# Kernel tuning notes

Measured on AMD Instinct MI355X. Metric: run time of the kernel, lower is better.

The kernel has to match this reference:

```python
import jax, jax.numpy as jnp
import numpy as np
from jax import lax

H_STEP = 1.0 / 3.0  # h = (t1 - t0) / N with t0=0, t1=1, N=3
N_STEPS = 3


def _conv(x, w):
    # x: [B, C, H, W], w: [O, I, kh, kw], 'same' padding, stride 1
    return lax.conv_general_dilated(
        x, w, window_strides=(1, 1), padding='SAME',
        dimension_numbers=('NCHW', 'OIHW', 'NCHW'))


def setup_inputs() -> dict:
    key = jax.random.key(0)
    ks = jax.random.split(key, 5)
    B, C, H, W = 16, 128, 128, 128
    fan_in = C * 9
    return {
        'x': jax.random.normal(ks[0], (B, C, H, W), dtype=jnp.float32),
        'w1': jax.random.normal(ks[1], (C, C, 3, 3), dtype=jnp.float32) * (2.0 / fan_in) ** 0.5,
        'b1': jax.random.normal(ks[2], (C,), dtype=jnp.float32) * 0.01,
        'w2': jax.random.normal(ks[3], (C, C, 3, 3), dtype=jnp.float32) * (2.0 / fan_in) ** 0.5,
        'b2': jax.random.normal(ks[4], (C,), dtype=jnp.float32) * 0.01,
    }


def reference(x, w1, b1, w2, b2):
    # Euler-step residual block: x <- x + h * conv2(relu(conv1(x))) for N steps
    for _ in range(N_STEPS):
        t = jax.nn.relu(_conv(x, w1) + b1[None, :, None, None])
        x = x + H_STEP * (_conv(t, w2) + b2[None, :, None, None])
    return jax.nn.relu(x)
```

## Files before the change

### kernel.cpp

```cpp
#include <hip/hip_runtime.h>
#include <hip/hip_bf16.h>


#define BATCH 16
#define CH    128
#define HH    128
#define WW    128
#define H_STEP (1.0f/3.0f)

#define CI_PAD 136

typedef short bf16x8 __attribute__((ext_vector_type(8)));
typedef float f32x4  __attribute__((ext_vector_type(4)));

__device__ __forceinline__ float bf2f(unsigned short u) {
    union { unsigned int i; float f; } c; c.i = ((unsigned int)u) << 16; return c.f;
}
__device__ __forceinline__ unsigned short f2bf(float f) {
    union { float f; unsigned int i; } c; c.f = f;
    unsigned int i = c.i;
    return (unsigned short)((i + 0x7FFFu + ((i >> 16) & 1u)) >> 16);
}

__global__ __launch_bounds__(256)
void transpose_x(const float* __restrict__ x, unsigned short* __restrict__ xb)
{
    __shared__ unsigned short s[128 * 132];
    const int tid = threadIdx.x;
    const int bz  = blockIdx.x;
    const int b = bz >> 7, y = bz & 127;

    #pragma unroll
    for (int it = 0; it < 16; ++it) {
        int idx = it * 256 + tid;
        int ci = idx >> 5, xq = idx & 31;
        float4 v = *(const float4*)&x[(((size_t)b * CH + ci) * HH + y) * WW + xq * 4];
        uint2 p;
        p.x = (unsigned int)f2bf(v.x) | ((unsigned int)f2bf(v.y) << 16);
        p.y = (unsigned int)f2bf(v.z) | ((unsigned int)f2bf(v.w) << 16);
        *(uint2*)&s[ci * 132 + xq * 4] = p;
    }
    __syncthreads();
    #pragma unroll
    for (int it = 0; it < 8; ++it) {
        int idx = it * 256 + tid;
        int xx = idx >> 4, cc = idx & 15;
        unsigned short t[8];
        #pragma unroll
        for (int k = 0; k < 8; ++k) t[k] = s[(cc * 8 + k) * 132 + xx];
        uint4 p;
        p.x = (unsigned int)t[0] | ((unsigned int)t[1] << 16);
        p.y = (unsigned int)t[2] | ((unsigned int)t[3] << 16);
        p.z = (unsigned int)t[4] | ((unsigned int)t[5] << 16);
        p.w = (unsigned int)t[6] | ((unsigned int)t[7] << 16);
        *(uint4*)&xb[((size_t)(b * HH + y) * WW + xx) * CH + cc * 8] = p;
    }
}

__global__ __launch_bounds__(256)
void convert_w(const float* __restrict__ w, unsigned short* __restrict__ wb)
{
    int idx = blockIdx.x * 256 + threadIdx.x;
    #pragma unroll
    for (int t = 0; t < 9; ++t)
        wb[t * 16384 + idx] = f2bf(w[(size_t)idx * 9 + t]);
}

template<int MODE>
__global__ __launch_bounds__(256, 2)
void conv_mfma(const unsigned short* __restrict__ in,
               const unsigned short* __restrict__ wb,
               const float* __restrict__ bias,
               const unsigned short* resb,
               unsigned short* outb,
               float* __restrict__ outf)
{
    __shared__ unsigned short s_in[130 * CI_PAD];
    __shared__ unsigned short s_w [128 * CI_PAD];

    const int tid = threadIdx.x;
    const int bz  = blockIdx.x;
    const int b = bz >> 7, y = bz & 127;

    const int lane = tid & 63;
    const int wid  = tid >> 6;
    const int woc0 = (wid >> 1) * 64;
    const int wpx0 = (wid & 1) * 64;
    const int n16  = lane & 15;
    const int q    = lane >> 4;

    f32x4 acc[4][4];
    #pragma unroll
    for (int i = 0; i < 4; ++i)
        #pragma unroll
        for (int j = 0; j < 4; ++j) acc[i][j] = (f32x4)0.0f;

    if (tid < 34) {
        int r  = (tid < 17) ? 0 : 129;
        int cc = (tid < 17) ? tid : tid - 17;
        uint4 z = {0u, 0u, 0u, 0u};
        *(uint4*)&s_in[r * CI_PAD + cc * 8] = z;
    }

    for (int ky = 0; ky < 3; ++ky) {
        const int gy = y + ky - 1;
        if (gy < 0 || gy >= HH) continue;
        const size_t inrow = ((size_t)(b * HH + gy) * WW) * CH;

        for (int kx = 0; kx < 3; ++kx) {
            __syncthreads();
            if (kx == 0) {
                #pragma unroll
                for (int it = 0; it < 8; ++it) {
                    int idx = it * 256 + tid;
                    int x = idx >> 4, cc = idx & 15;
                    uint4 v = *(const uint4*)&in[inrow + (size_t)x * CH + cc * 8];
                    *(uint4*)&s_in[(x + 1) * CI_PAD + cc * 8] = v;
                }
            }
            const unsigned short* wt = wb + (ky * 3 + kx) * 16384;
            #pragma unroll
            for (int it = 0; it < 8; ++it) {
                int idx = it * 256 + tid;
                int oc = idx >> 4, cc = idx & 15;
                uint4 v = *(const uint4*)&wt[oc * 128 + cc * 8];
                *(uint4*)&s_w[oc * CI_PAD + cc * 8] = v;
            }
            __syncthreads();

            #pragma unroll
            for (int c0 = 0; c0 < 128; c0 += 32) {
                bf16x8 af[4], bfr[4];
                #pragma unroll
                for (int i = 0; i < 4; ++i)
                    af[i] = *(const bf16x8*)&s_w[(woc0 + i * 16 + n16) * CI_PAD + c0 + q * 8];
                #pragma unroll
                for (int j = 0; j < 4; ++j)
                    bfr[j] = *(const bf16x8*)&s_in[(wpx0 + j * 16 + n16 + kx) * CI_PAD + c0 + q * 8];
                #pragma unroll
                for (int i = 0; i < 4; ++i)
                    #pragma unroll
                    for (int j = 0; j < 4; ++j)
                        acc[i][j] = __builtin_amdgcn_mfma_f32_16x16x32_bf16(
                            af[i], bfr[j], acc[i][j], 0, 0, 0);
            }
        }
    }

    const int ybase = (b * HH + y) * WW;
    if (MODE == 0 || MODE == 1) {
        #pragma unroll
        for (int j = 0; j < 4; ++j) {
            int x = wpx0 + j * 16 + n16;
            size_t pbase = (size_t)(ybase + x) * CH;
            #pragma unroll
            for (int i = 0; i < 4; ++i) {
                int oc0 = woc0 + i * 16 + q * 4;
                float v0 = acc[i][j][0] + bias[oc0 + 0];
                float v1 = acc[i][j][1] + bias[oc0 + 1];
                float v2 = acc[i][j][2] + bias[oc0 + 2];
                float v3 = acc[i][j][3] + bias[oc0 + 3];
                if (MODE == 0) {
                    v0 = fmaxf(v0, 0.f); v1 = fmaxf(v1, 0.f);
                    v2 = fmaxf(v2, 0.f); v3 = fmaxf(v3, 0.f);
                } else {
                    uint2 rr = *(const uint2*)&resb[pbase + oc0];
                    v0 = bf2f((unsigned short)(rr.x & 0xffff)) + H_STEP * v0;
                    v1 = bf2f((unsigned short)(rr.x >> 16))    + H_STEP * v1;
                    v2 = bf2f((unsigned short)(rr.y & 0xffff)) + H_STEP * v2;
                    v3 = bf2f((unsigned short)(rr.y >> 16))    + H_STEP * v3;
                }
                uint2 po;
                po.x = (unsigned int)f2bf(v0) | ((unsigned int)f2bf(v1) << 16);
                po.y = (unsigned int)f2bf(v2) | ((unsigned int)f2bf(v3) << 16);
                *(uint2*)&outb[pbase + oc0] = po;
            }
        }
    } else {
        #pragma unroll
        for (int i = 0; i < 4; ++i) {
            #pragma unroll
            for (int r = 0; r < 4; ++r) {
                int oc = woc0 + i * 16 + q * 4 + r;
                float bv = bias[oc];
                size_t orow = ((size_t)(b * CH + oc) * HH + y) * WW;
                #pragma unroll
                for (int j = 0; j < 4; ++j) {
                    int x = wpx0 + j * 16 + n16;
                    float v = acc[i][j][r] + bv;
                    v = bf2f(resb[(size_t)(ybase + x) * CH + oc]) + H_STEP * v;
                    outf[orow + x] = fmaxf(v, 0.f);
                }
            }
        }
    }
}

extern "C" void kernel_launch(void* const* d_in, const int* in_sizes, int n_in,
                              void* d_out, int out_size, void* d_ws, size_t ws_size,
                              hipStream_t stream) {
    const float* x0 = (const float*)d_in[0];
    const float* w1 = (const float*)d_in[1];
    const float* b1 = (const float*)d_in[2];
    const float* w2 = (const float*)d_in[3];
    const float* b2 = (const float*)d_in[4];

    const size_t NELEM = (size_t)BATCH * CH * HH * WW;
    unsigned short* XB = (unsigned short*)d_ws;
    unsigned short* T  = XB + NELEM;

    unsigned short* WB1;
    if (ws_size >= NELEM * 4 + 2 * 294912)
        WB1 = T + NELEM;
    else
        WB1 = (unsigned short*)d_in[0];
    unsigned short* WB2 = WB1 + 9 * 16384;

    dim3 block(256);
    dim3 gridRow(BATCH * HH);

    transpose_x<<<gridRow, block, 0, stream>>>(x0, XB);
    convert_w<<<dim3(64), block, 0, stream>>>(w1, WB1);
    convert_w<<<dim3(64), block, 0, stream>>>(w2, WB2);

    conv_mfma<0><<<gridRow, block, 0, stream>>>(XB, WB1, b1, nullptr, T, nullptr);
    conv_mfma<1><<<gridRow, block, 0, stream>>>(T, WB2, b2, XB, XB, nullptr);
    conv_mfma<0><<<gridRow, block, 0, stream>>>(XB, WB1, b1, nullptr, T, nullptr);
    conv_mfma<1><<<gridRow, block, 0, stream>>>(T, WB2, b2, XB, XB, nullptr);
    conv_mfma<0><<<gridRow, block, 0, stream>>>(XB, WB1, b1, nullptr, T, nullptr);
    conv_mfma<2><<<gridRow, block, 0, stream>>>(T, WB2, b2, XB, nullptr, (float*)d_out);
}
```

Before: 795.7 us.

## Restructure conv to 2-row tiles with 32x32 MFMA and direct-to-LDS loads

Each block now computes two output rows and loops over input-channel groups of 16, staging all 9 taps of weights and 4 input rows in LDS at once, so weights and input rows are reused across both rows and all taps. It switches from 16x16x32 to 32x32x16 bf16 MFMA, changes the weight layout to match the new LDS tiling, and uses global_load_lds to copy straight into LDS without going through registers. The cost is more barriers per block (eight channel-group iterations) with no double buffering. Padding is removed from the LDS layout, which may cause bank conflicts.

After: 1.006 ms. 1.26x slower.

```diff
diff --git a/kernel.cpp b/kernel.cpp
--- a/kernel.cpp
+++ b/kernel.cpp
@@ -8,10 +8,8 @@
 #define WW    128
 #define H_STEP (1.0f/3.0f)
 
-#define CI_PAD 136
-
 typedef short bf16x8 __attribute__((ext_vector_type(8)));
-typedef float f32x4  __attribute__((ext_vector_type(4)));
+typedef float f32x16 __attribute__((ext_vector_type(16)));
 
 __device__ __forceinline__ float bf2f(unsigned short u) {
     union { unsigned int i; float f; } c; c.i = ((unsigned int)u) << 16; return c.f;
@@ -20,6 +18,12 @@
     union { float f; unsigned int i; } c; c.f = f;
     unsigned int i = c.i;
     return (unsigned short)((i + 0x7FFFu + ((i >> 16) & 1u)) >> 16);
+}
+
+__device__ __forceinline__ void gload_lds16(const void* g, void* l) {
+    __builtin_amdgcn_global_load_lds(
+        (const __attribute__((address_space(1))) unsigned int*)g,
+        (__attribute__((address_space(3))) unsigned int*)l, 16, 0, 0);
 }
 
 __global__ __launch_bounds__(256)
@@ -61,9 +65,12 @@
 void convert_w(const float* __restrict__ w, unsigned short* __restrict__ wb)
 {
     int idx = blockIdx.x * 256 + threadIdx.x;
+    int oc = idx >> 7, ci = idx & 127;
+    int c0g = ci >> 4, h = (ci >> 3) & 1, cc = ci & 7;
     #pragma unroll
     for (int t = 0; t < 9; ++t)
-        wb[t * 16384 + idx] = f2bf(w[(size_t)idx * 9 + t]);
+        wb[(((((size_t)c0g * 9 + t) * 2 + h) * 128 + oc) * 8) + cc]
+            = f2bf(w[(size_t)idx * 9 + t]);
 }
 
 template<int MODE>
@@ -75,121 +82,145 @@
                unsigned short* outb,
                float* __restrict__ outf)
 {
-    __shared__ unsigned short s_in[130 * CI_PAD];
-    __shared__ unsigned short s_w [128 * CI_PAD];
-
-    const int tid = threadIdx.x;
-    const int bz  = blockIdx.x;
-    const int b = bz >> 7, y = bz & 127;
+    __shared__ unsigned short s_w[9 * 2 * 128 * 8];
+    __shared__ unsigned short s_in[2 * 4 * 130 * 8];
+
+    const int tid  = threadIdx.x;
+    const int bz   = blockIdx.x;
+    const int b    = bz >> 6;
+    const int y0   = (bz & 63) * 2;
 
     const int lane = tid & 63;
     const int wid  = tid >> 6;
-    const int woc0 = (wid >> 1) * 64;
-    const int wpx0 = (wid & 1) * 64;
-    const int n16  = lane & 15;
-    const int q    = lane >> 4;
-
-    f32x4 acc[4][4];
+    const int rw   = wid >> 1;
+    const int xw   = (wid & 1) * 64;
+    const int n    = lane & 31;
+    const int h    = lane >> 5;
+
+    if (tid < 16) {
+        int hh2 = tid >> 3, rrs = (tid >> 1) & 3, sl = (tid & 1) ? 129 : 0;
+        uint4 z = {0u, 0u, 0u, 0u};
+        *(uint4*)&s_in[((hh2 * 4 + rrs) * 130 + sl) * 8] = z;
+    }
+    {
+        int bad_rs = (y0 == 0) ? 0 : ((y0 == 126) ? 3 : -1);
+        if (bad_rs >= 0) {
+            for (int i2 = tid; i2 < 2 * 130; i2 += 256) {
+                int hh2 = i2 / 130, sl = i2 % 130;
+                uint4 z = {0u, 0u, 0u, 0u};
+                *(uint4*)&s_in[((hh2 * 4 + bad_rs) * 130 + sl) * 8] = z;
+            }
+        }
+    }
+
+    f32x16 acc[4][2];
     #pragma unroll
     for (int i = 0; i < 4; ++i)
         #pragma unroll
-        for (int j = 0; j < 4; ++j) acc[i][j] = (f32x4)0.0f;
-
-    if (tid < 34) {
-        int r  = (tid < 17) ? 0 : 129;
-        int cc = (tid < 17) ? tid : tid - 17;
-        uint4 z = {0u, 0u, 0u, 0u};
-        *(uint4*)&s_in[r * CI_PAD + cc * 8] = z;
-    }
-
-    for (int ky = 0; ky < 3; ++ky) {
-        const int gy = y + ky - 1;
-        if (gy < 0 || gy >= HH) continue;
-        const size_t inrow = ((size_t)(b * HH + gy) * WW) * CH;
-
-        for (int kx = 0; kx < 3; ++kx) {
-            __syncthreads();
-            if (kx == 0) {
-                #pragma unroll
-                for (int it = 0; it < 8; ++it) {
-                    int idx = it * 256 + tid;
-                    int x = idx >> 4, cc = idx & 15;
-                    uint4 v = *(const uint4*)&in[inrow + (size_t)x * CH + cc * 8];
-                    *(uint4*)&s_in[(x + 1) * CI_PAD + cc * 8] = v;
+        for (int j = 0; j < 2; ++j) acc[i][j] = (f32x16)0.0f;
+
+    const int  my_gy    = y0 + wid - 1;
+    const bool my_valid = (my_gy >= 0) && (my_gy < HH);
+    const char* inrow   = (const char*)(in + ((size_t)(b * HH + my_gy) * WW) * CH);
+    const char* wbc     = (const char*)wb;
+
+    for (int c0g = 0; c0g < 8; ++c0g) {
+        __syncthreads();
+        {
+            const char* gsrc = wbc + c0g * 36864 + wid * 9216;
+            char*       ldst = (char*)s_w + wid * 9216;
+            #pragma unroll
+            for (int it = 0; it < 9; ++it)
+                gload_lds16(gsrc + it * 1024 + lane * 16,
+                            ldst + it * 1024 + lane * 16);
+        }
+        if (my_valid) {
+            #pragma unroll
+            for (int hh2 = 0; hh2 < 2; ++hh2)
+                #pragma unroll
+                for (int half = 0; half < 2; ++half) {
+                    int x = half * 64 + lane;
+                    gload_lds16(inrow + (size_t)x * 256 + c0g * 32 + hh2 * 16,
+                                (char*)&s_in[((hh2 * 4 + wid) * 130 + 1 + half * 64) * 8]
+                                    + lane * 16);
                 }
-            }
-            const unsigned short* wt = wb + (ky * 3 + kx) * 16384;
-            #pragma unroll
-            for (int it = 0; it < 8; ++it) {
-                int idx = it * 256 + tid;
-                int oc = idx >> 4, cc = idx & 15;
-                uint4 v = *(const uint4*)&wt[oc * 128 + cc * 8];
-                *(uint4*)&s_w[oc * CI_PAD + cc * 8] = v;
-            }
-            __syncthreads();
-
-            #pragma unroll
-            for (int c0 = 0; c0 < 128; c0 += 32) {
-                bf16x8 af[4], bfr[4];
+        }
+        __syncthreads();
+
+        #pragma unroll
+        for (int ky = 0; ky < 3; ++ky) {
+            const int rs = rw + ky;
+            #pragma unroll
+            for (int kx = 0; kx < 3; ++kx) {
+                const int tap = ky * 3 + kx;
+                bf16x8 af[4], bfr[2];
                 #pragma unroll
                 for (int i = 0; i < 4; ++i)
-                    af[i] = *(const bf16x8*)&s_w[(woc0 + i * 16 + n16) * CI_PAD + c0 + q * 8];
-                #pragma unroll
-                for (int j = 0; j < 4; ++j)
-                    bfr[j] = *(const bf16x8*)&s_in[(wpx0 + j * 16 + n16 + kx) * CI_PAD + c0 + q * 8];
+                    af[i] = *(const bf16x8*)&s_w[((tap * 2 + h) * 128 + i * 32 + n) * 8];
+                #pragma unroll
+                for (int j = 0; j < 2; ++j)
+                    bfr[j] = *(const bf16x8*)&s_in[((h * 4 + rs) * 130 + xw + j * 32 + n + kx) * 8];
                 #pragma unroll
                 for (int i = 0; i < 4; ++i)
                     #pragma unroll
-                    for (int j = 0; j < 4; ++j)
-                        acc[i][j] = __builtin_amdgcn_mfma_f32_16x16x32_bf16(
+                    for (int j = 0; j < 2; ++j)
+                        acc[i][j] = __builtin_amdgcn_mfma_f32_32x32x16_bf16(
                             af[i], bfr[j], acc[i][j], 0, 0, 0);
             }
         }
     }
 
-    const int ybase = (b * HH + y) * WW;
+    const int y_r = y0 + rw;
     if (MODE == 0 || MODE == 1) {
         #pragma unroll
-        for (int j = 0; j < 4; ++j) {
-            int x = wpx0 + j * 16 + n16;
-            size_t pbase = (size_t)(ybase + x) * CH;
+        for (int j = 0; j < 2; ++j) {
+            const int x = xw + j * 32 + n;
+            const size_t pbase = ((size_t)(b * HH + y_r) * WW + x) * CH;
             #pragma unroll
             for (int i = 0; i < 4; ++i) {
-                int oc0 = woc0 + i * 16 + q * 4;
-                float v0 = acc[i][j][0] + bias[oc0 + 0];
-                float v1 = acc[i][j][1] + bias[oc0 + 1];
-                float v2 = acc[i][j][2] + bias[oc0 + 2];
-                float v3 = acc[i][j][3] + bias[oc0 + 3];
-                if (MODE == 0) {
-                    v0 = fmaxf(v0, 0.f); v1 = fmaxf(v1, 0.f);
-                    v2 = fmaxf(v2, 0.f); v3 = fmaxf(v3, 0.f);
-                } else {
-                    uint2 rr = *(const uint2*)&resb[pbase + oc0];
-                    v0 = bf2f((unsigned short)(rr.x & 0xffff)) + H_STEP * v0;
-                    v1 = bf2f((unsigned short)(rr.x >> 16))    + H_STEP * v1;
-                    v2 = bf2f((unsigned short)(rr.y & 0xffff)) + H_STEP * v2;
-                    v3 = bf2f((unsigned short)(rr.y >> 16))    + H_STEP * v3;
+                #pragma unroll
+                for (int a = 0; a < 4; ++a) {
+                    const int oc0 = i * 32 + a * 8 + h * 4;
+                    float4 bv = *(const float4*)&bias[oc0];
+                    float v0 = acc[i][j][a * 4 + 0] + bv.x;
+                    float v1 = acc[i][j][a * 4 + 1] + bv.y;
+                    float v2 = acc[i][j][a * 4 + 2] + bv.z;
+                    float v3 = acc[i][j][a * 4 + 3] + bv.w;
+                    if (MODE == 0) {
+                        v0 = fmaxf(v0, 0.f); v1 = fmaxf(v1, 0.f);
+                        v2 = fmaxf(v2, 0.f); v3 = fmaxf(v3, 0.f);
+                    } else {
+                        uint2 rr = *(const uint2*)&resb[pbase + oc0];
+                        v0 = bf2f((unsigned short)(rr.x & 0xffff)) + H_STEP * v0;
+                        v1 = bf2f((unsigned short)(rr.x >> 16))    + H_STEP * v1;
+                        v2 = bf2f((unsigned short)(rr.y & 0xffff)) + H_STEP * v2;
+                        v3 = bf2f((unsigned short)(rr.y >> 16))    + H_STEP * v3;
+                    }
+                    uint2 po;
+                    po.x = (unsigned int)f2bf(v0) | ((unsigned int)f2bf(v1) << 16);
+                    po.y = (unsigned int)f2bf(v2) | ((unsigned int)f2bf(v3) << 16);
+                    *(uint2*)&outb[pbase + oc0] = po;
                 }
-                uint2 po;
-                po.x = (unsigned int)f2bf(v0) | ((unsigned int)f2bf(v1) << 16);
-                po.y = (unsigned int)f2bf(v2) | ((unsigned int)f2bf(v3) << 16);
-                *(uint2*)&outb[pbase + oc0] = po;
             }
         }
     } else {
         #pragma unroll
         for (int i = 0; i < 4; ++i) {
             #pragma unroll
-            for (int r = 0; r < 4; ++r) {
-                int oc = woc0 + i * 16 + q * 4 + r;
-                float bv = bias[oc];
-                size_t orow = ((size_t)(b * CH + oc) * HH + y) * WW;
-                #pragma unroll
-                for (int j = 0; j < 4; ++j) {
-                    int x = wpx0 + j * 16 + n16;
-                    float v = acc[i][j][r] + bv;
-                    v = bf2f(resb[(size_t)(ybase + x) * CH + oc]) + H_STEP * v;
-                    outf[orow + x] = fmaxf(v, 0.f);
+            for (int a = 0; a < 4; ++a) {
+                #pragma unroll
+                for (int r = 0; r < 4; ++r) {
+                    const int oc = i * 32 + a * 8 + h * 4 + r;
+                    const float bv = bias[oc];
+                    const size_t orow = ((size_t)(b * CH + oc) * HH + y_r) * WW;
+                    #pragma unroll
+                    for (int j = 0; j < 2; ++j) {
+                        const int x = xw + j * 32 + n;
+                        float v = acc[i][j][a * 4 + r] + bv;
+                        v = bf2f(resb[((size_t)(b * HH + y_r) * WW + x) * CH + oc])
+                            + H_STEP * v;
+                        outf[orow + x] = fmaxf(v, 0.f);
+                    }
                 }
             }
         }
@@ -217,16 +248,17 @@
     unsigned short* WB2 = WB1 + 9 * 16384;
 
     dim3 block(256);
-    dim3 gridRow(BATCH * HH);
-
-    transpose_x<<<gridRow, block, 0, stream>>>(x0, XB);
+    dim3 gridT(BATCH * HH);
+    dim3 gridC(BATCH * (HH / 2));
+
+    transpose_x<<<gridT, block, 0, stream>>>(x0, XB);
     convert_w<<<dim3(64), block, 0, stream>>>(w1, WB1);
     convert_w<<<dim3(64), block, 0, stream>>>(w2, WB2);
 
-    conv_mfma<0><<<gridRow, block, 0, stream>>>(XB, WB1, b1, nullptr, T, nullptr);
-    conv_mfma<1><<<gridRow, block, 0, stream>>>(T, WB2, b2, XB, XB, nullptr);
-    conv_mfma<0><<<gridRow, block, 0, stream>>>(XB, WB1, b1, nullptr, T, nullptr);
-    conv_mfma<1><<<gridRow, block, 0, stream>>>(T, WB2, b2, XB, XB, nullptr);
-    conv_mfma<0><<<gridRow, block, 0, stream>>>(XB, WB1, b1, nullptr, T, nullptr);
-    conv_mfma<2><<<gridRow, block, 0, stream>>>(T, WB2, b2, XB, nullptr, (float*)d_out);
-}
+    conv_mfma<0><<<gridC, block, 0, stream>>>(XB, WB1, b1, nullptr, T, nullptr);
+    conv_mfma<1><<<gridC, block, 0, stream>>>(T, WB2, b2, XB, XB, nullptr);
+    conv_mfma<0><<<gridC, block, 0, stream>>>(XB, WB1, b1, nullptr, T, nullptr);
+    conv_mfma<1><<<gridC, block, 0, stream>>>(T, WB2, b2, XB, XB, nullptr);
+    conv_mfma<0><<<gridC, block, 0, stream>>>(XB, WB1, b1, nullptr, T, nullptr);
+    conv_mfma<2><<<gridC, block, 0, stream>>>(T, WB2, b2, XB, nullptr, (float*)d_out);
+}
```
